# Performance work log

Measured on AMD Instinct MI355X. Metric: run time of the kernel, lower is better.

## Reference

```python
import jax, jax.numpy as jnp
import numpy as np

GAMMA = 1.4
N_PTS, N_IC, HID = 32768, 16384, 128


def _mlp(layers, p):
    # tanh MLP; layers = list of (W, b), last layer linear
    h = p
    for W, b in layers[:-1]:
        h = jnp.tanh(h @ W + b)
    W, b = layers[-1]
    return h @ W + b


def setup_inputs() -> dict:
    key = jax.random.key(0)
    ks = jax.random.split(key, 16)
    d = {
        "x_train": jax.random.uniform(ks[0], (N_PTS, 3), jnp.float32),
        "x_initial": jax.random.uniform(ks[1], (N_IC, 3), jnp.float32),
        "ic": jax.random.uniform(ks[2], (4, 4), jnp.float32),
    }
    def lin(k, fi, fo):
        return jax.random.normal(k, (fi, fo), jnp.float32) * np.float32(np.sqrt(1.0 / fi))
    dims_m = [(3, HID), (HID, HID), (HID, HID), (HID, 4)]
    dims_n = [(3, HID), (HID, HID), (HID, HID), (HID, 1)]
    for i, (fi, fo) in enumerate(dims_m):
        d[f"mw{i}"] = lin(ks[3 + i], fi, fo)
        d[f"mb{i}"] = jnp.zeros((fo,), jnp.float32)
    for i, (fi, fo) in enumerate(dims_n):
        d[f"nw{i}"] = lin(ks[8 + i], fi, fo)
        d[f"nb{i}"] = jnp.zeros((fo,), jnp.float32)
    return d


def _loss(x_train, x_initial, ic,
          mw0, mb0, mw1, mb1, mw2, mb2, mw3, mb3,
          nw0, nb0, nw1, nb1, nw2, nb2, nw3, nb3):
    layers_m = [(mw0, mb0), (mw1, mb1), (mw2, mb2), (mw3, mb3)]
    layers_n = [(nw0, nb0), (nw1, nb1), (nw2, nb2), (nw3, nb3)]

    def prim(p):  # p: (3,) = (x, y, t)
        o = _mlp(layers_m, p)
        rho, pr, u, v = o[0], o[1], o[2], o[3]
        E = pr / (GAMMA - 1.0) + 0.5 * rho * (u * u + v * v)
        return rho, pr, u, v, E

    def Ufn(p):  # conserved state U1..U4
        rho, pr, u, v, E = prim(p)
        return jnp.stack([rho, rho * u, rho * v, E])

    def quant(p):  # [U1..U4, f1..f4, g1..g4]
        rho, pr, u, v, E = prim(p)
        U = jnp.stack([rho, rho * u, rho * v, E])
        f = jnp.stack([rho * u, rho * u * u + pr, rho * u * v, u * (E + pr)])
        g = jnp.stack([rho * v, rho * u * v, rho * v * v + pr, v * (E + pr)])
        return jnp.concatenate([U, f, g])

    # one fused forward-mode Jacobian sweep replaces 20 torch autograd.grad calls
    J = jax.vmap(jax.jacfwd(quant))(x_train)            # (N, 12, 3)
    Hs = jax.vmap(jax.jacfwd(jax.jacfwd(Ufn)))(x_train)  # (N, 4, 3, 3)

    mu = 0.01 * jnp.squeeze(_mlp(layers_n, x_train), -1) ** 2  # (N,)
    lap = Hs[:, :, 0, 0] + Hs[:, :, 1, 1]               # U_xx + U_yy, (N, 4)
    # res_i = U_i_t + f_i_x + g_i_y - mu * (U_i_xx + U_i_yy)
    res = J[:, 0:4, 2] + J[:, 4:8, 0] + J[:, 8:12, 1] - mu[:, None] * lap
    r = jnp.mean(res ** 2, axis=0)                      # (4,) -> r1..r4

    # initial-condition quadrant loss (masked means, jit-safe)
    pred = _mlp(layers_m, x_initial)                    # (Ni, 4)
    xl = x_initial[:, 0] < 0.5
    xr = x_initial[:, 0] > 0.5
    yt = x_initial[:, 1] > 0.5
    yb = x_initial[:, 1] < 0.5
    perm = jnp.array([0, 3, 1, 2])  # ic columns -> [rho, p, u, v] target order
    init_loss = jnp.float32(0.0)
    for row, mask in ((1, xl & yt), (3, xr & yt), (0, xl & yb), (2, xr & yb)):
        tgt = ic[row][perm]                             # (4,)
        m = mask.astype(pred.dtype)
        denom = jnp.maximum(jnp.sum(m), 1.0)
        init_loss = init_loss + jnp.sum(m[:, None] * (pred - tgt) ** 2) / denom

    return jnp.sum(r) + 10.0 * init_loss + 0.1 * jnp.mean(mu ** 2)


def reference(x_train, x_initial, ic,
              mw0, mb0, mw1, mb1, mw2, mb2, mw3, mb3,
              nw0, nb0, nw1, nb1, nw2, nb2, nw3, nb3):
    return _loss(x_train, x_initial, ic,
                 mw0, mb0, mw1, mb1, mw2, mb2, mw3, mb3,
                 nw0, nb0, nw1, nb1, nw2, nb2, nw3, nb3)
```

## Files before the change

### kernel.cpp

```cpp
#include <hip/hip_runtime.h>

#define NPTS 32768
#define NIC  16384
#define GRID 512
#define BLK  256
#define NW   4

typedef __attribute__((ext_vector_type(8))) _Float16 f16x8;
typedef __attribute__((ext_vector_type(4))) float f32x4;

#define SWZ(e, r) ((e) ^ (((r) & 7) << 3))
#define MFMA16 __builtin_amdgcn_mfma_f32_16x16x32_f16
#define VMCNT0 asm volatile("s_waitcnt vmcnt(0)" ::: "memory")

__device__ __forceinline__ float tanh_fast(float x) {
    float e = __expf(2.0f * x);
    return 1.0f - 2.0f / (e + 1.0f);
}

__device__ __forceinline__ float wave_allsum(float v) {
#pragma unroll
    for (int off = 32; off > 0; off >>= 1) v += __shfl_xor(v, off, 64);
    return v;
}

__device__ __forceinline__ unsigned short f2hb(float x) {
    return __builtin_bit_cast(unsigned short, (_Float16)x);
}
__device__ __forceinline__ uint2 pack4h(float a, float b, float c, float d) {
    return make_uint2((unsigned)f2hb(a) | ((unsigned)f2hb(b) << 16),
                      (unsigned)f2hb(c) | ((unsigned)f2hb(d) << 16));
}

__device__ __forceinline__ void stage_w_async(const unsigned short* __restrict__ src,
                                              _Float16* dst, int tid) {
    const unsigned int* gp = (const unsigned int*)src;
    unsigned int* lp = (unsigned int*)dst;
#pragma unroll
    for (int k = 0; k < 8; k++) {
        __builtin_amdgcn_global_load_lds(
            (const __attribute__((address_space(1))) unsigned int*)(gp + (tid + k * BLK) * 4),
            (__attribute__((address_space(3))) unsigned int*)(lp + (tid + k * BLK) * 4),
            16, 0, 0);
    }
}

__global__ __launch_bounds__(512) void k_prep(
    const float* __restrict__ mw1, const float* __restrict__ mw2,
    const float* __restrict__ nw1, const float* __restrict__ nw2,
    const float* __restrict__ mw3,
    unsigned short* __restrict__ wt1, unsigned short* __restrict__ wt2,
    unsigned short* __restrict__ nt1, unsigned short* __restrict__ nt2,
    unsigned short* __restrict__ w3t) {
    const int tid = threadIdx.x;
    const int bk = blockIdx.x;
    if (bk == 4) {
        for (int i = tid; i < 2048; i += 512) w3t[i] = 0;
        __syncthreads();
        if (tid < 512) {
            const int j = tid & 127, k = tid >> 7;
            w3t[k * 128 + SWZ(j, k)] = f2hb(mw3[j * 4 + k]);
        }
        return;
    }
    const float* src = (bk == 0) ? mw1 : (bk == 1) ? mw2 : (bk == 2) ? nw1 : nw2;
    unsigned short* dst = (bk == 0) ? wt1 : (bk == 1) ? wt2 : (bk == 2) ? nt1 : nt2;
    __shared__ float sM[128 * 129];
#pragma unroll
    for (int k = 0; k < 32; k++) {
        const int idx = tid + k * 512;
        const int j = idx >> 7, n = idx & 127;
        sM[n * 129 + j] = src[idx];
    }
    __syncthreads();
#pragma unroll
    for (int k = 0; k < 32; k++) {
        const int d = tid + k * 512;
        const int n = d >> 7, js = d & 127;
        const int j = js ^ ((n & 7) << 3);
        dst[d] = f2hb(sM[n * 129 + j]);
    }
}

template <int PT>
__device__ __forceinline__ void hidden_val(const _Float16* sW, _Float16* sHv,
                                           const float* bias,
                                           const unsigned short* nextW, _Float16* sWdst,
                                           int tid, int wv, int g, int l15) {
    f32x4 acc[2][PT];
#pragma unroll
    for (int rr = 0; rr < 2; rr++)
#pragma unroll
        for (int pt = 0; pt < PT; pt++) acc[rr][pt] = (f32x4){0.f, 0.f, 0.f, 0.f};
#pragma unroll
    for (int ks = 0; ks < 4; ks++) {
        const int ee = SWZ(ks * 32 + g * 8, l15);
        const f16x8 A0 = *(const f16x8*)&sW[(wv * 32 + l15) * 128 + ee];
        const f16x8 A1 = *(const f16x8*)&sW[(wv * 32 + 16 + l15) * 128 + ee];
#pragma unroll
        for (int pt = 0; pt < PT; pt++) {
            const f16x8 Bv = *(const f16x8*)&sHv[(pt * 16 + l15) * 128 + ee];
            acc[0][pt] = MFMA16(A0, Bv, acc[0][pt], 0, 0, 0);
            acc[1][pt] = MFMA16(A1, Bv, acc[1][pt], 0, 0, 0);
        }
    }
    __syncthreads();
    if (nextW) stage_w_async(nextW, sWdst, tid);
    float hv[2][PT][4];
#pragma unroll
    for (int rr = 0; rr < 2; rr++)
#pragma unroll
        for (int pt = 0; pt < PT; pt++)
#pragma unroll
            for (int r = 0; r < 4; r++) {
                const int n = wv * 32 + rr * 16 + g * 4 + r;
                hv[rr][pt][r] = tanh_fast(acc[rr][pt][r] + bias[n]);
            }
#pragma unroll
    for (int rr = 0; rr < 2; rr++)
#pragma unroll
        for (int pt = 0; pt < PT; pt++) {
            const int row = pt * 16 + l15;
            *(uint2*)&sHv[row * 128 + SWZ(wv * 32 + rr * 16 + g * 4, row)] =
                pack4h(hv[rr][pt][0], hv[rr][pt][1], hv[rr][pt][2], hv[rr][pt][3]);
        }
}

__device__ __forceinline__ void hidden_res(const _Float16* sW, _Float16* sH6,
                                           const float* bias,
                                           const unsigned short* nextW, _Float16* sWdst,
                                           int tid, int wv, int g, int l15) {
    f32x4 acc[2][6];
#pragma unroll
    for (int rr = 0; rr < 2; rr++)
#pragma unroll
        for (int c = 0; c < 6; c++) acc[rr][c] = (f32x4){0.f, 0.f, 0.f, 0.f};
#pragma unroll
    for (int ks = 0; ks < 4; ks++) {
        const int ee = SWZ(ks * 32 + g * 8, l15);
        const f16x8 A0 = *(const f16x8*)&sW[(wv * 32 + l15) * 128 + ee];
        const f16x8 A1 = *(const f16x8*)&sW[(wv * 32 + 16 + l15) * 128 + ee];
#pragma unroll
        for (int c = 0; c < 6; c++) {
            const f16x8 Bv = *(const f16x8*)&sH6[c * 2048 + l15 * 128 + ee];
            acc[0][c] = MFMA16(A0, Bv, acc[0][c], 0, 0, 0);
            acc[1][c] = MFMA16(A1, Bv, acc[1][c], 0, 0, 0);
        }
    }
    __syncthreads();
    if (nextW) stage_w_async(nextW, sWdst, tid);
    float ch[2][6][4];
#pragma unroll
    for (int rr = 0; rr < 2; rr++)
#pragma unroll
        for (int r = 0; r < 4; r++) {
            const int n = wv * 32 + rr * 16 + g * 4 + r;
            const float z0 = acc[rr][0][r] + bias[n];
            const float a = tanh_fast(z0);
            const float s = 1.f - a * a;
            const float zx = acc[rr][1][r], zy = acc[rr][2][r];
            ch[rr][0][r] = a;
            ch[rr][1][r] = s * zx;
            ch[rr][2][r] = s * zy;
            ch[rr][3][r] = s * acc[rr][3][r];
            ch[rr][4][r] = s * acc[rr][4][r] - 2.f * a * s * zx * zx;
            ch[rr][5][r] = s * acc[rr][5][r] - 2.f * a * s * zy * zy;
        }
#pragma unroll
    for (int rr = 0; rr < 2; rr++) {
        const int eo = l15 * 128 + SWZ(wv * 32 + rr * 16 + g * 4, l15);
#pragma unroll
        for (int c = 0; c < 6; c++)
            *(uint2*)&sH6[c * 2048 + eo] =
                pack4h(ch[rr][c][0], ch[rr][c][1], ch[rr][c][2], ch[rr][c][3]);
    }
}

__global__ __launch_bounds__(BLK) void k_fused(
    const float* __restrict__ xtr, const float* __restrict__ xin,
    const float* __restrict__ icg,
    const float* __restrict__ mw0, const float* __restrict__ mb0,
    const float* __restrict__ mb1, const float* __restrict__ mb2,
    const float* __restrict__ mb3,
    const float* __restrict__ nw0, const float* __restrict__ nb0,
    const float* __restrict__ nb1, const float* __restrict__ nb2,
    const float* __restrict__ nw3, const float* __restrict__ nb3,
    const unsigned short* __restrict__ wt1, const unsigned short* __restrict__ wt2,
    const unsigned short* __restrict__ nt1, const unsigned short* __restrict__ nt2,
    const unsigned short* __restrict__ w3t,
    float* __restrict__ resPart, float* __restrict__ muPart,
    float* __restrict__ icPart) {
    __shared__ __align__(16) _Float16 sW[16384];
    __shared__ __align__(16) _Float16 sH[6 * 2048];
    __shared__ __align__(16) _Float16 sA[2048];
    __shared__ __align__(16) float sO[384];
    __shared__ float sB[520];
    __shared__ float sMu[64];
    __shared__ float sTq[16];
    __shared__ float sRed[NW][8];

    const int tid = threadIdx.x;
    const int lane = tid & 63, wv = tid >> 6;
    const int g = lane >> 4, l15 = lane & 15;
    const int p16 = tid & 15, chunk = tid >> 4;

    stage_w_async(nt1, sW, tid);
    if (tid < 128) { sB[tid] = mb1[tid]; sB[260 + tid] = nb1[tid]; }
    else           { sB[tid] = mb2[tid - 128]; sB[260 + tid] = nb2[tid - 128]; }
    if (tid < 4) sB[256 + tid] = mb3[tid];
    if (tid == 4) sB[516] = nb3[0];
    if (tid < 16) {
        const int k = tid & 3, q = tid >> 2;
        const int row = (q == 0) ? 1 : ((q == 1) ? 3 : ((q == 2) ? 0 : 2));
        const int pc = (k == 0) ? 0 : ((k == 1) ? 3 : ((k == 2) ? 1 : 2));
        sTq[q * 4 + k] = icg[row * 4 + pc];
    }
    for (int i = tid; i < 2048; i += BLK) sA[i] = (_Float16)0.f;
    if (tid < 128) sA[tid] = (_Float16)nw3[tid];

    float wxr[8], wyr[8], wzr[8], wbr[8];
#pragma unroll
    for (int j = 0; j < 8; j++) {
        const int n = chunk * 8 + j;
        wxr[j] = nw0[n]; wyr[j] = nw0[128 + n]; wzr[j] = nw0[256 + n]; wbr[j] = nb0[n];
    }

    float accMu2 = 0.f;
    {
        const int pt0 = blockIdx.x * 64;
        const int ee0 = SWZ(chunk * 8, p16);
#pragma unroll
        for (int pp = 0; pp < 4; pp++) {
            const int p = pt0 + pp * 16 + p16;
            const float x = xtr[p * 3 + 0], y = xtr[p * 3 + 1], t = xtr[p * 3 + 2];
            float hv[8];
#pragma unroll
            for (int j = 0; j < 8; j++)
                hv[j] = tanh_fast(fmaf(wxr[j], x, fmaf(wyr[j], y, fmaf(wzr[j], t, wbr[j]))));
            const uint2 lo = pack4h(hv[0], hv[1], hv[2], hv[3]);
            const uint2 hi = pack4h(hv[4], hv[5], hv[6], hv[7]);
            *(uint4*)&sH[(pp * 16 + p16) * 128 + ee0] = make_uint4(lo.x, lo.y, hi.x, hi.y);
        }
        VMCNT0; __syncthreads();
        hidden_val<4>(sW, sH, &sB[260], nt2, sW, tid, wv, g, l15);
        VMCNT0; __syncthreads();
        hidden_val<4>(sW, sH, &sB[388], wt1, sW, tid, wv, g, l15);
        __syncthreads();
        {
            f32x4 a4 = (f32x4){0.f, 0.f, 0.f, 0.f};
#pragma unroll
            for (int ks = 0; ks < 4; ks++) {
                const int ee = SWZ(ks * 32 + g * 8, l15);
                const f16x8 Af = *(const f16x8*)&sA[l15 * 128 + ee];
                const f16x8 Bv = *(const f16x8*)&sH[(wv * 16 + l15) * 128 + ee];
                a4 = MFMA16(Af, Bv, a4, 0, 0, 0);
            }
            if (g == 0) {
                const float o = a4[0] + sB[516];
                const float muv = 0.01f * o * o;
                sMu[wv * 16 + l15] = muv;
                accMu2 += muv * muv;
            }
        }
        __syncthreads();
    }
    accMu2 = wave_allsum(accMu2);
    if (lane == 0) sRed[wv][0] = accMu2;
    __syncthreads();
    if (tid == 0)
        muPart[blockIdx.x] = sRed[0][0] + sRed[1][0] + sRed[2][0] + sRed[3][0];

#pragma unroll
    for (int j = 0; j < 8; j++) {
        const int n = chunk * 8 + j;
        wxr[j] = mw0[n]; wyr[j] = mw0[128 + n]; wzr[j] = mw0[256 + n]; wbr[j] = mb0[n];
    }

    {
        const int pt0 = blockIdx.x * 32;
        const int ee0 = SWZ(chunk * 8, p16);
#pragma unroll
        for (int pp = 0; pp < 2; pp++) {
            const int p = pt0 + pp * 16 + p16;
            const float x = xin[p * 3 + 0], y = xin[p * 3 + 1], t = xin[p * 3 + 2];
            float hv[8];
#pragma unroll
            for (int j = 0; j < 8; j++)
                hv[j] = tanh_fast(fmaf(wxr[j], x, fmaf(wyr[j], y, fmaf(wzr[j], t, wbr[j]))));
            const uint2 lo = pack4h(hv[0], hv[1], hv[2], hv[3]);
            const uint2 hi = pack4h(hv[4], hv[5], hv[6], hv[7]);
            *(uint4*)&sH[(pp * 16 + p16) * 128 + ee0] = make_uint4(lo.x, lo.y, hi.x, hi.y);
        }
        VMCNT0; __syncthreads();
        hidden_val<2>(sW, sH, &sB[0], wt2, sW, tid, wv, g, l15);
        ((uint4*)sA)[tid] = ((const uint4*)w3t)[tid];
        VMCNT0; __syncthreads();
        hidden_val<2>(sW, sH, &sB[128], wt1, sW, tid, wv, g, l15);
        __syncthreads();
        float qs[4] = {0, 0, 0, 0}, qc[4] = {0, 0, 0, 0};
        if (wv < 2) {
            f32x4 a4 = (f32x4){0.f, 0.f, 0.f, 0.f};
#pragma unroll
            for (int ks = 0; ks < 4; ks++) {
                const int ee = SWZ(ks * 32 + g * 8, l15);
                const f16x8 Af = *(const f16x8*)&sA[l15 * 128 + ee];
                const f16x8 Bv = *(const f16x8*)&sH[(wv * 16 + l15) * 128 + ee];
                a4 = MFMA16(Af, Bv, a4, 0, 0, 0);
            }
            if (g == 0) {
                const int p = pt0 + wv * 16 + l15;
                const float o0 = a4[0] + sB[256];
                const float o1 = a4[1] + sB[257];
                const float o2 = a4[2] + sB[258];
                const float o3 = a4[3] + sB[259];
                const float x = xin[p * 3 + 0];
                const float y = xin[p * 3 + 1];
                int quad = -1;
                if (x < 0.5f && y > 0.5f) quad = 0;
                else if (x > 0.5f && y > 0.5f) quad = 1;
                else if (x < 0.5f && y < 0.5f) quad = 2;
                else if (x > 0.5f && y < 0.5f) quad = 3;
                if (quad >= 0) {
                    const float d0 = o0 - sTq[quad * 4 + 0];
                    const float d1 = o1 - sTq[quad * 4 + 1];
                    const float d2 = o2 - sTq[quad * 4 + 2];
                    const float d3 = o3 - sTq[quad * 4 + 3];
                    const float ss = d0 * d0 + d1 * d1 + d2 * d2 + d3 * d3;
#pragma unroll
                    for (int qq = 0; qq < 4; qq++) {
                        qs[qq] += (quad == qq) ? ss : 0.f;
                        qc[qq] += (quad == qq) ? 1.f : 0.f;
                    }
                }
            }
        }
        __syncthreads();
#pragma unroll
        for (int qq = 0; qq < 4; qq++) {
            qs[qq] = wave_allsum(qs[qq]);
            qc[qq] = wave_allsum(qc[qq]);
        }
        if (lane == 0) {
#pragma unroll
            for (int qq = 0; qq < 4; qq++) { sRed[wv][qq] = qs[qq]; sRed[wv][4 + qq] = qc[qq]; }
        }
        __syncthreads();
        if (tid == 0) {
#pragma unroll
            for (int q = 0; q < 8; q++)
                icPart[blockIdx.x * 8 + q] =
                    sRed[0][q] + sRed[1][q] + sRed[2][q] + sRed[3][q];
        }
        __syncthreads();
    }

    float racc0 = 0.f, racc1 = 0.f, racc2 = 0.f, racc3 = 0.f;
    const int base = blockIdx.x * 64;
    for (int b = 0; b < 4; b++) {
        const int pt0 = base + b * 16;
        {
            const int p = pt0 + p16;
            const float x = xtr[p * 3 + 0], y = xtr[p * 3 + 1], t = xtr[p * 3 + 2];
            float ch[6][8];
#pragma unroll
            for (int j = 0; j < 8; j++) {
                const float z = fmaf(wxr[j], x, fmaf(wyr[j], y, fmaf(wzr[j], t, wbr[j])));
                const float a = tanh_fast(z);
                const float s = 1.f - a * a;
                ch[0][j] = a;
                ch[1][j] = s * wxr[j];
                ch[2][j] = s * wyr[j];
                ch[3][j] = s * wzr[j];
                ch[4][j] = -2.f * a * s * wxr[j] * wxr[j];
                ch[5][j] = -2.f * a * s * wyr[j] * wyr[j];
            }
            const int off = p16 * 128 + SWZ(chunk * 8, p16);
#pragma unroll
            for (int c = 0; c < 6; c++) {
                const uint2 lo = pack4h(ch[c][0], ch[c][1], ch[c][2], ch[c][3]);
                const uint2 hi = pack4h(ch[c][4], ch[c][5], ch[c][6], ch[c][7]);
                *(uint4*)&sH[c * 2048 + off] = make_uint4(lo.x, lo.y, hi.x, hi.y);
            }
        }
        VMCNT0; __syncthreads();
        hidden_res(sW, sH, &sB[0], wt2, sW, tid, wv, g, l15);
        VMCNT0; __syncthreads();
        hidden_res(sW, sH, &sB[128],
                   (b < 3) ? wt1 : (const unsigned short*)nullptr, sW, tid, wv, g, l15);
        __syncthreads();
#pragma unroll
        for (int tt = 0; tt < 2; tt++) {
            const int c = wv + tt * 4;
            if (c < 6) {
                f32x4 a4 = (f32x4){0.f, 0.f, 0.f, 0.f};
#pragma unroll
                for (int ks = 0; ks < 4; ks++) {
                    const int ee = SWZ(ks * 32 + g * 8, l15);
                    const f16x8 Af = *(const f16x8*)&sA[l15 * 128 + ee];
                    const f16x8 Bf = *(const f16x8*)&sH[c * 2048 + l15 * 128 + ee];
                    a4 = MFMA16(Af, Bf, a4, 0, 0, 0);
                }
                if (g == 0) {
                    float4 o = make_float4(a4[0], a4[1], a4[2], a4[3]);
                    if (c == 0) { o.x += sB[256]; o.y += sB[257]; o.z += sB[258]; o.w += sB[259]; }
                    *(float4*)&sO[(c * 16 + l15) * 4] = o;
                }
            }
        }
        __syncthreads();
        if (wv == 0) {
            const int pp = lane & 15;
            const float m = sMu[b * 16 + pp];
            float oq[4][6];
#pragma unroll
            for (int c = 0; c < 6; c++) {
                const float4 o = *(const float4*)&sO[(c * 16 + pp) * 4];
                oq[0][c] = o.x; oq[1][c] = o.y; oq[2][c] = o.z; oq[3][c] = o.w;
            }
            const float rho = oq[0][0], rho_x = oq[0][1], rho_y = oq[0][2],
                        rho_t = oq[0][3], rho_xx = oq[0][4], rho_yy = oq[0][5];
            const float pr = oq[1][0], pr_x = oq[1][1], pr_y = oq[1][2],
                        pr_t = oq[1][3], pr_xx = oq[1][4], pr_yy = oq[1][5];
            const float u = oq[2][0], u_x = oq[2][1], u_y = oq[2][2],
                        u_t = oq[2][3], u_xx = oq[2][4], u_yy = oq[2][5];
            const float v = oq[3][0], v_x = oq[3][1], v_y = oq[3][2],
                        v_t = oq[3][3], v_xx = oq[3][4], v_yy = oq[3][5];

            const float ig1 = 2.5f;
            const float ke = 0.5f * (u * u + v * v);
            const float E = pr * ig1 + rho * ke;
            const float d_x = u * u_x + v * v_x;
            const float d_y = u * u_y + v * v_y;
            const float d_t = u * u_t + v * v_t;
            const float E_x = pr_x * ig1 + rho_x * ke + rho * d_x;
            const float E_y = pr_y * ig1 + rho_y * ke + rho * d_y;
            const float E_t = pr_t * ig1 + rho_t * ke + rho * d_t;
            const float E_xx = pr_xx * ig1 + rho_xx * ke + 2.f * rho_x * d_x +
                               rho * (u_x * u_x + u * u_xx + v_x * v_x + v * v_xx);
            const float E_yy = pr_yy * ig1 + rho_yy * ke + 2.f * rho_y * d_y +
                               rho * (u_y * u_y + u * u_yy + v_y * v_y + v * v_yy);

            const float r1 = rho_t + (rho_x * u + rho * u_x) + (rho_y * v + rho * v_y)
                           - m * (rho_xx + rho_yy);
            const float r2 = (rho_t * u + rho * u_t)
                           + (rho_x * u * u + 2.f * rho * u * u_x + pr_x)
                           + (rho_y * u * v + rho * u_y * v + rho * u * v_y)
                           - m * ((rho_xx * u + 2.f * rho_x * u_x + rho * u_xx)
                                + (rho_yy * u + 2.f * rho_y * u_y + rho * u_yy));
            const float r3 = (rho_t * v + rho * v_t)
                           + (rho_x * u * v + rho * u_x * v + rho * u * v_x)
                           + (rho_y * v * v + 2.f * rho * v * v_y + pr_y)
                           - m * ((rho_xx * v + 2.f * rho_x * v_x + rho * v_xx)
                                + (rho_yy * v + 2.f * rho_y * v_y + rho * v_yy));
            const float r4 = E_t
                           + (u_x * (E + pr) + u * (E_x + pr_x))
                           + (v_y * (E + pr) + v * (E_y + pr_y))
                           - m * (E_xx + E_yy);
            if (lane < 16) {
                racc0 += r1 * r1; racc1 += r2 * r2;
                racc2 += r3 * r3; racc3 += r4 * r4;
            }
        }
        __syncthreads();
    }

    if (wv == 0) {
        racc0 = wave_allsum(racc0);
        racc1 = wave_allsum(racc1);
        racc2 = wave_allsum(racc2);
        racc3 = wave_allsum(racc3);
        if (lane == 0) {
            resPart[blockIdx.x * 4 + 0] = racc0;
            resPart[blockIdx.x * 4 + 1] = racc1;
            resPart[blockIdx.x * 4 + 2] = racc2;
            resPart[blockIdx.x * 4 + 3] = racc3;
        }
    }
}

__global__ void k_fin(const float* __restrict__ resPart, const float* __restrict__ muPart,
                      const float* __restrict__ icPart, float* __restrict__ out) {
    const int lane = threadIdx.x;
    float r[4] = {0, 0, 0, 0};
    float m2 = 0.f;
    float qs[4] = {0, 0, 0, 0}, qc[4] = {0, 0, 0, 0};
    for (int b = lane; b < GRID; b += 64) {
#pragma unroll
        for (int i = 0; i < 4; i++) r[i] += resPart[b * 4 + i];
        m2 += muPart[b];
#pragma unroll
        for (int q = 0; q < 4; q++) {
            qs[q] += icPart[b * 8 + q];
            qc[q] += icPart[b * 8 + 4 + q];
        }
    }
#pragma unroll
    for (int i = 0; i < 4; i++) r[i] = wave_allsum(r[i]);
    m2 = wave_allsum(m2);
#pragma unroll
    for (int q = 0; q < 4; q++) { qs[q] = wave_allsum(qs[q]); qc[q] = wave_allsum(qc[q]); }
    if (lane == 0) {
        const float sumr = (r[0] + r[1] + r[2] + r[3]) / (float)NPTS;
        float init_loss = 0.f;
#pragma unroll
        for (int q = 0; q < 4; q++) init_loss += qs[q] / fmaxf(qc[q], 1.f);
        out[0] = sumr + 10.f * init_loss + 0.1f * (m2 / (float)NPTS);
    }
}

extern "C" void kernel_launch(void* const* d_in, const int* in_sizes, int n_in,
                              void* d_out, int out_size, void* d_ws, size_t ws_size,
                              hipStream_t stream) {
    const float* xtr = (const float*)d_in[0];
    const float* xin = (const float*)d_in[1];
    const float* icg = (const float*)d_in[2];
    const float* mw0 = (const float*)d_in[3];
    const float* mb0 = (const float*)d_in[4];
    const float* mw1 = (const float*)d_in[5];
    const float* mb1 = (const float*)d_in[6];
    const float* mw2 = (const float*)d_in[7];
    const float* mb2 = (const float*)d_in[8];
    const float* mw3 = (const float*)d_in[9];
    const float* mb3 = (const float*)d_in[10];
    const float* nw0 = (const float*)d_in[11];
    const float* nb0 = (const float*)d_in[12];
    const float* nw1 = (const float*)d_in[13];
    const float* nb1 = (const float*)d_in[14];
    const float* nw2 = (const float*)d_in[15];
    const float* nb2 = (const float*)d_in[16];
    const float* nw3 = (const float*)d_in[17];
    const float* nb3 = (const float*)d_in[18];

    float* wsf = (float*)d_ws;
    float* resPart = wsf;
    float* muPart = wsf + 2048;
    float* icPart = wsf + 2560;
    unsigned short* wt1 = (unsigned short*)(wsf + 6656);
    unsigned short* wt2 = wt1 + 16384;
    unsigned short* nt1 = wt2 + 16384;
    unsigned short* nt2 = nt1 + 16384;
    unsigned short* w3t = nt2 + 16384;

    k_prep<<<5, 512, 0, stream>>>(mw1, mw2, nw1, nw2, mw3, wt1, wt2, nt1, nt2, w3t);
    k_fused<<<GRID, BLK, 0, stream>>>(xtr, xin, icg,
                                      mw0, mb0, mb1, mb2, mb3,
                                      nw0, nb0, nb1, nb2, nw3, nb3,
                                      wt1, wt2, nt1, nt2, w3t,
                                      resPart, muPart, icPart);
    k_fin<<<1, 64, 0, stream>>>(resPart, muPart, icPart, (float*)d_out);
}
```

Baseline: 58.89 us.

## Keep hidden-layer weight fragments in registers instead of restaging through LDS

Each wave now loads its A-operand fragments for both hidden layers straight from global memory into registers once per network, instead of asynchronously restaging each 128x128 weight matrix into shared memory before every layer. This removes the repeated LDS staging traffic and the vmcnt waits between layers, and frees 32 KB of shared memory per block, which may allow more resident blocks. In exchange each thread holds 16 extra f16x8 vectors, which raises register pressure and may lower occupancy or cause spills.

Result: slower. 71.02 us (+20.6%).

```diff
diff --git a/kernel.cpp b/kernel.cpp
--- a/kernel.cpp
+++ b/kernel.cpp
@@ -11,7 +11,6 @@
 
 #define SWZ(e, r) ((e) ^ (((r) & 7) << 3))
 #define MFMA16 __builtin_amdgcn_mfma_f32_16x16x32_f16
-#define VMCNT0 asm volatile("s_waitcnt vmcnt(0)" ::: "memory")
 
 __device__ __forceinline__ float tanh_fast(float x) {
     float e = __expf(2.0f * x);
@@ -30,19 +29,6 @@
 __device__ __forceinline__ uint2 pack4h(float a, float b, float c, float d) {
     return make_uint2((unsigned)f2hb(a) | ((unsigned)f2hb(b) << 16),
                       (unsigned)f2hb(c) | ((unsigned)f2hb(d) << 16));
-}
-
-__device__ __forceinline__ void stage_w_async(const unsigned short* __restrict__ src,
-                                              _Float16* dst, int tid) {
-    const unsigned int* gp = (const unsigned int*)src;
-    unsigned int* lp = (unsigned int*)dst;
-#pragma unroll
-    for (int k = 0; k < 8; k++) {
-        __builtin_amdgcn_global_load_lds(
-            (const __attribute__((address_space(1))) unsigned int*)(gp + (tid + k * BLK) * 4),
-            (__attribute__((address_space(3))) unsigned int*)(lp + (tid + k * BLK) * 4),
-            16, 0, 0);
-    }
 }
 
 __global__ __launch_bounds__(512) void k_prep(
@@ -83,10 +69,8 @@
 }
 
 template <int PT>
-__device__ __forceinline__ void hidden_val(const _Float16* sW, _Float16* sHv,
-                                           const float* bias,
-                                           const unsigned short* nextW, _Float16* sWdst,
-                                           int tid, int wv, int g, int l15) {
+__device__ __forceinline__ void hidden_val(const f16x8 (&aW)[2][4], _Float16* sHv,
+                                           const float* bias, int wv, int g, int l15) {
     f32x4 acc[2][PT];
 #pragma unroll
     for (int rr = 0; rr < 2; rr++)
@@ -95,17 +79,14 @@
 #pragma unroll
     for (int ks = 0; ks < 4; ks++) {
         const int ee = SWZ(ks * 32 + g * 8, l15);
-        const f16x8 A0 = *(const f16x8*)&sW[(wv * 32 + l15) * 128 + ee];
-        const f16x8 A1 = *(const f16x8*)&sW[(wv * 32 + 16 + l15) * 128 + ee];
 #pragma unroll
         for (int pt = 0; pt < PT; pt++) {
             const f16x8 Bv = *(const f16x8*)&sHv[(pt * 16 + l15) * 128 + ee];
-            acc[0][pt] = MFMA16(A0, Bv, acc[0][pt], 0, 0, 0);
-            acc[1][pt] = MFMA16(A1, Bv, acc[1][pt], 0, 0, 0);
+            acc[0][pt] = MFMA16(aW[0][ks], Bv, acc[0][pt], 0, 0, 0);
+            acc[1][pt] = MFMA16(aW[1][ks], Bv, acc[1][pt], 0, 0, 0);
         }
     }
     __syncthreads();
-    if (nextW) stage_w_async(nextW, sWdst, tid);
     float hv[2][PT][4];
 #pragma unroll
     for (int rr = 0; rr < 2; rr++)
@@ -126,10 +107,8 @@
         }
 }
 
-__device__ __forceinline__ void hidden_res(const _Float16* sW, _Float16* sH6,
-                                           const float* bias,
-                                           const unsigned short* nextW, _Float16* sWdst,
-                                           int tid, int wv, int g, int l15) {
+__device__ __forceinline__ void hidden_res(const f16x8 (&aW)[2][4], _Float16* sH6,
+                                           const float* bias, int wv, int g, int l15) {
     f32x4 acc[2][6];
 #pragma unroll
     for (int rr = 0; rr < 2; rr++)
@@ -138,17 +117,14 @@
 #pragma unroll
     for (int ks = 0; ks < 4; ks++) {
         const int ee = SWZ(ks * 32 + g * 8, l15);
-        const f16x8 A0 = *(const f16x8*)&sW[(wv * 32 + l15) * 128 + ee];
-        const f16x8 A1 = *(const f16x8*)&sW[(wv * 32 + 16 + l15) * 128 + ee];
 #pragma unroll
         for (int c = 0; c < 6; c++) {
             const f16x8 Bv = *(const f16x8*)&sH6[c * 2048 + l15 * 128 + ee];
-            acc[0][c] = MFMA16(A0, Bv, acc[0][c], 0, 0, 0);
-            acc[1][c] = MFMA16(A1, Bv, acc[1][c], 0, 0, 0);
+            acc[0][c] = MFMA16(aW[0][ks], Bv, acc[0][c], 0, 0, 0);
+            acc[1][c] = MFMA16(aW[1][ks], Bv, acc[1][c], 0, 0, 0);
         }
     }
     __syncthreads();
-    if (nextW) stage_w_async(nextW, sWdst, tid);
     float ch[2][6][4];
 #pragma unroll
     for (int rr = 0; rr < 2; rr++)
@@ -190,7 +166,6 @@
     const unsigned short* __restrict__ w3t,
     float* __restrict__ resPart, float* __restrict__ muPart,
     float* __restrict__ icPart) {
-    __shared__ __align__(16) _Float16 sW[16384];
     __shared__ __align__(16) _Float16 sH[6 * 2048];
     __shared__ __align__(16) _Float16 sA[2048];
     __shared__ __align__(16) float sO[384];
@@ -204,7 +179,20 @@
     const int g = lane >> 4, l15 = lane & 15;
     const int p16 = tid & 15, chunk = tid >> 4;
 
-    stage_w_async(nt1, sW, tid);
+    f16x8 aW[2][2][4];
+    const int arow0 = (wv * 32 + l15) * 128;
+    const int arow1 = (wv * 32 + 16 + l15) * 128;
+    {
+#pragma unroll
+        for (int ks = 0; ks < 4; ks++) {
+            const int ee = SWZ(ks * 32 + g * 8, l15);
+            aW[0][0][ks] = *(const f16x8*)&nt1[arow0 + ee];
+            aW[0][1][ks] = *(const f16x8*)&nt1[arow1 + ee];
+            aW[1][0][ks] = *(const f16x8*)&nt2[arow0 + ee];
+            aW[1][1][ks] = *(const f16x8*)&nt2[arow1 + ee];
+        }
+    }
+
     if (tid < 128) { sB[tid] = mb1[tid]; sB[260 + tid] = nb1[tid]; }
     else           { sB[tid] = mb2[tid - 128]; sB[260 + tid] = nb2[tid - 128]; }
     if (tid < 4) sB[256 + tid] = mb3[tid];
@@ -241,10 +229,10 @@
             const uint2 hi = pack4h(hv[4], hv[5], hv[6], hv[7]);
             *(uint4*)&sH[(pp * 16 + p16) * 128 + ee0] = make_uint4(lo.x, lo.y, hi.x, hi.y);
         }
-        VMCNT0; __syncthreads();
-        hidden_val<4>(sW, sH, &sB[260], nt2, sW, tid, wv, g, l15);
-        VMCNT0; __syncthreads();
-        hidden_val<4>(sW, sH, &sB[388], wt1, sW, tid, wv, g, l15);
+        __syncthreads();
+        hidden_val<4>(aW[0], sH, &sB[260], wv, g, l15);
+        __syncthreads();
+        hidden_val<4>(aW[1], sH, &sB[388], wv, g, l15);
         __syncthreads();
         {
             f32x4 a4 = (f32x4){0.f, 0.f, 0.f, 0.f};
@@ -275,6 +263,15 @@
         const int n = chunk * 8 + j;
         wxr[j] = mw0[n]; wyr[j] = mw0[128 + n]; wzr[j] = mw0[256 + n]; wbr[j] = mb0[n];
     }
+#pragma unroll
+    for (int ks = 0; ks < 4; ks++) {
+        const int ee = SWZ(ks * 32 + g * 8, l15);
+        aW[0][0][ks] = *(const f16x8*)&wt1[arow0 + ee];
+        aW[0][1][ks] = *(const f16x8*)&wt1[arow1 + ee];
+        aW[1][0][ks] = *(const f16x8*)&wt2[arow0 + ee];
+        aW[1][1][ks] = *(const f16x8*)&wt2[arow1 + ee];
+    }
+    ((uint4*)sA)[tid] = ((const uint4*)w3t)[tid];
 
     {
         const int pt0 = blockIdx.x * 32;
@@ -291,11 +288,10 @@
             const uint2 hi = pack4h(hv[4], hv[5], hv[6], hv[7]);
             *(uint4*)&sH[(pp * 16 + p16) * 128 + ee0] = make_uint4(lo.x, lo.y, hi.x, hi.y);
         }
-        VMCNT0; __syncthreads();
-        hidden_val<2>(sW, sH, &sB[0], wt2, sW, tid, wv, g, l15);
-        ((uint4*)sA)[tid] = ((const uint4*)w3t)[tid];
-        VMCNT0; __syncthreads();
-        hidden_val<2>(sW, sH, &sB[128], wt1, sW, tid, wv, g, l15);
+        __syncthreads();
+        hidden_val<2>(aW[0], sH, &sB[0], wv, g, l15);
+        __syncthreads();
+        hidden_val<2>(aW[1], sH, &sB[128], wv, g, l15);
         __syncthreads();
         float qs[4] = {0, 0, 0, 0}, qc[4] = {0, 0, 0, 0};
         if (wv < 2) {
@@ -382,11 +378,10 @@
                 *(uint4*)&sH[c * 2048 + off] = make_uint4(lo.x, lo.y, hi.x, hi.y);
             }
         }
-        VMCNT0; __syncthreads();
-        hidden_res(sW, sH, &sB[0], wt2, sW, tid, wv, g, l15);
-        VMCNT0; __syncthreads();
-        hidden_res(sW, sH, &sB[128],
-                   (b < 3) ? wt1 : (const unsigned short*)nullptr, sW, tid, wv, g, l15);
+        __syncthreads();
+        hidden_res(aW[0], sH, &sB[0], wv, g, l15);
+        __syncthreads();
+        hidden_res(aW[1], sH, &sB[128], wv, g, l15);
         __syncthreads();
 #pragma unroll
         for (int tt = 0; tt < 2; tt++) {
```
